# Performance work log

Hardware: AMD Instinct MI355X
Metric: run time of the kernel (lower is better)

## Reference

```python
import jax, jax.numpy as jnp
import numpy as np

F_THRESHOLD = 10  # zero out DCT coefficients with i + j <= 10 (low-frequency triangle)


def _dct_mat(N):
    # torch_dct.dct with norm=None: X_k = 2 * sum_n x_n cos(pi*(2n+1)*k/(2N))
    n = np.arange(N)
    k = np.arange(N)[:, None]
    return (2.0 * np.cos(np.pi * (2 * n + 1) * k / (2 * N))).astype(np.float32)  # [k, n]


def _idct_mat(N):
    # inverse of the norm=None DCT-II above: x_n = (1/N) * sum_k w_k X_k cos(pi*(2n+1)*k/(2N)), w_0=0.5
    n = np.arange(N)[:, None]
    k = np.arange(N)
    w = np.ones(N, dtype=np.float64)
    w[0] = 0.5
    return ((w * np.cos(np.pi * (2 * n + 1) * k / (2 * N))) / N).astype(np.float32)  # [n, k]


def _filtermask(H, W):
    i = jnp.arange(H)[:, None]
    j = jnp.arange(W)[None, :]
    return jnp.where(i + j <= F_THRESHOLD, 0.0, 1.0).astype(jnp.float32)  # [H, W]


def setup_inputs() -> dict:
    key = jax.random.key(0)
    im = jax.random.normal(key, (32, 3, 512, 512), dtype=jnp.float32)
    return {"im": im}


def reference(im) -> jnp.ndarray:
    B, C, H, W = im.shape
    Ch = jnp.asarray(_dct_mat(H))   # [kh, h]
    Cw = jnp.asarray(_dct_mat(W))   # [kw, w]
    Dh = jnp.asarray(_idct_mat(H))  # [h, kh]
    Dw = jnp.asarray(_idct_mat(W))  # [w, kw]
    mask = _filtermask(H, W)

    # dct_2d: DCT-II along W then along H
    x = jnp.einsum('kh,bchw,lw->bckl', Ch, im, Cw)
    x = x * mask  # zero low-frequency triangle
    # idct_2d
    x = jnp.einsum('hk,bckl,wl->bchw', Dh, x, Dw)
    return x
```

## Files before the change

### kernel.cpp

```cpp
#include <hip/hip_runtime.h>
#include <math.h>

#define NPIX 512
#define NK 11
#define NKP 12
#define NPAIR 121
#define RBLKS 8
#define NCH 96

typedef float vfloat4 __attribute__((ext_vector_type(4)));

#if __has_builtin(__builtin_amdgcn_cosf)
__device__ inline float cos_rev(float rev) { return __builtin_amdgcn_cosf(rev); }
#else
__device__ inline float cos_rev(float rev) { return __cosf(rev * 6.28318530717958647692f); }
#endif

__device__ inline float ctab(int h, int k) {
    int m = ((2 * h + 1) * k) & 2047;
    return 2.0f * cos_rev((float)m * (1.0f / 2048.0f));
}

#if __has_builtin(__builtin_amdgcn_update_dpp)
template <int CTRL>
__device__ inline float dpp_add(float x) {
    int xi = __builtin_bit_cast(int, x);
    int yi = __builtin_amdgcn_update_dpp(0, xi, CTRL, 0xf, 0xf, false);
    return x + __builtin_bit_cast(float, yi);
}
__device__ inline float red16(float x) {
    x = dpp_add<0x128>(x);
    x = dpp_add<0x124>(x);
    x = dpp_add<0x122>(x);
    x = dpp_add<0x121>(x);
    return x;
}
#else
__device__ inline float red16(float x) {
    x += __shfl_xor(x, 8);
    x += __shfl_xor(x, 4);
    x += __shfl_xor(x, 2);
    x += __shfl_xor(x, 1);
    return x;
}
#endif

__device__ inline void build_Cs64(float (*Cs64)[NKP], int t, int row0) {
#pragma unroll
    for (int j = 0; j < 3; ++j) {
        int idx = j * 256 + t;
        int hl = idx / NKP;
        int kk = idx - hl * NKP;
        Cs64[hl][kk] = (kk < NK) ? ctab(row0 + hl, kk) : 0.f;
    }
}

#define FMA4(ACC, CC) ACC.x += (CC) * v.x; ACC.y += (CC) * v.y; ACC.z += (CC) * v.z; ACC.w += (CC) * v.w;
#define DOT4(ACC) ((ACC).x * cl0 + (ACC).y * cl1 + (ACC).z * cl2 + (ACC).w * cl3)

__global__ __launch_bounds__(256, 4) void k_partial(const float* __restrict__ im,
                                                    float* __restrict__ plow) {
    __shared__ float Cs64[64][NKP];
    __shared__ float red[16][NPAIR];

    int bid = blockIdx.x;
    int c = bid >> 3, rb = bid & 7;
    int t = threadIdx.x;
    int row0 = rb * 64;

    build_Cs64(Cs64, t, row0);
    __syncthreads();

    int half = t >> 7;
    int col4 = t & 127;
    int w0 = col4 * 4;
    int hbase = half * 32;
    const float* imc = im + (size_t)c * NPIX * NPIX + (size_t)(row0 + hbase) * NPIX + w0;

    float4 z = make_float4(0.f, 0.f, 0.f, 0.f);
    float4 a0 = z, a1 = z, a2 = z, a3 = z, a4 = z, a5 = z, a6 = z, a7 = z, a8 = z, a9 = z, a10 = z;

#pragma unroll 4
    for (int i = 0; i < 32; ++i) {
        float4 v = *(const float4*)(imc + (size_t)i * NPIX);
        const float4* crow = (const float4*)&Cs64[hbase + i][0];
        float4 c0 = crow[0], c1 = crow[1], c2 = crow[2];
        FMA4(a0, c0.x) FMA4(a1, c0.y) FMA4(a2, c0.z) FMA4(a3, c0.w)
        FMA4(a4, c1.x) FMA4(a5, c1.y) FMA4(a6, c1.z) FMA4(a7, c1.w)
        FMA4(a8, c2.x) FMA4(a9, c2.y) FMA4(a10, c2.z)
    }

    int g = t >> 4;
    for (int l = 0; l < NK; ++l) {
        float cl0 = ctab(w0 + 0, l);
        float cl1 = ctab(w0 + 1, l);
        float cl2 = ctab(w0 + 2, l);
        float cl3 = ctab(w0 + 3, l);
        float p0 = red16(DOT4(a0));
        float p1 = red16(DOT4(a1));
        float p2 = red16(DOT4(a2));
        float p3 = red16(DOT4(a3));
        float p4 = red16(DOT4(a4));
        float p5 = red16(DOT4(a5));
        float p6 = red16(DOT4(a6));
        float p7 = red16(DOT4(a7));
        float p8 = red16(DOT4(a8));
        float p9 = red16(DOT4(a9));
        float p10 = red16(DOT4(a10));
        if ((t & 15) == 0) {
            red[g][0 * NK + l] = p0;  red[g][1 * NK + l] = p1;  red[g][2 * NK + l] = p2;
            red[g][3 * NK + l] = p3;  red[g][4 * NK + l] = p4;  red[g][5 * NK + l] = p5;
            red[g][6 * NK + l] = p6;  red[g][7 * NK + l] = p7;  red[g][8 * NK + l] = p8;
            red[g][9 * NK + l] = p9;  red[g][10 * NK + l] = p10;
        }
    }
    __syncthreads();

    if (t < NPAIR) {
        float s = 0.f;
#pragma unroll
        for (int gg = 0; gg < 16; ++gg) s += red[gg][t];
        plow[(size_t)bid * NPAIR + t] = s;
    }
}

__global__ __launch_bounds__(256, 2) void k_output(const float* __restrict__ im,
                                                   const float* __restrict__ plow,
                                                   float* __restrict__ out) {
    __shared__ float Cs64[64][NKP];
    __shared__ float Ls[NPAIR];

    int bid = blockIdx.x;
    int c = bid >> 3, rb = bid & 7;
    int t = threadIdx.x;
    int row0 = rb * 64;

    build_Cs64(Cs64, t, row0);

    if (t < NPAIR) {
        int k = t / NK, l = t % NK;
        float s = 0.f;
        const float* pp = plow + (size_t)c * RBLKS * NPAIR + t;
#pragma unroll
        for (int b = 0; b < RBLKS; ++b) s += pp[b * NPAIR];
        float sk = (k == 0 ? 0.5f : 1.0f) * (1.0f / 1024.0f);
        float sl = (l == 0 ? 0.5f : 1.0f) * (1.0f / 1024.0f);
        Ls[t] = (k + l <= 10) ? s * sk * sl : 0.f;
    }
    __syncthreads();

    int half = t >> 7;
    int col4 = t & 127;
    int w0 = col4 * 4;
    int hbase = half * 32;

    float4 z = make_float4(0.f, 0.f, 0.f, 0.f);
    float4 B0 = z, B1 = z, B2 = z, B3 = z, B4 = z, B5 = z, B6 = z, B7 = z, B8 = z, B9 = z, B10 = z;

#define BADD(BK, KI) { float lw = Ls[(KI) * NK + l]; BK.x += lw * cl0; BK.y += lw * cl1; BK.z += lw * cl2; BK.w += lw * cl3; }
    for (int l = 0; l < NK; ++l) {
        float cl0 = ctab(w0 + 0, l);
        float cl1 = ctab(w0 + 1, l);
        float cl2 = ctab(w0 + 2, l);
        float cl3 = ctab(w0 + 3, l);
        BADD(B0, 0) BADD(B1, 1) BADD(B2, 2) BADD(B3, 3) BADD(B4, 4) BADD(B5, 5)
        BADD(B6, 6) BADD(B7, 7) BADD(B8, 8) BADD(B9, 9) BADD(B10, 10)
    }

    const float* imc = im + (size_t)c * NPIX * NPIX + (size_t)(row0 + hbase) * NPIX + w0;
    float* outc = out + (size_t)c * NPIX * NPIX + (size_t)(row0 + hbase) * NPIX + w0;

#define CORR(comp) (c0.x * B0.comp + c0.y * B1.comp + c0.z * B2.comp + c0.w * B3.comp \
                  + c1.x * B4.comp + c1.y * B5.comp + c1.z * B6.comp + c1.w * B7.comp \
                  + c2.x * B8.comp + c2.y * B9.comp + c2.z * B10.comp)

#pragma unroll 4
    for (int i = 0; i < 32; ++i) {
        float4 v = *(const float4*)(imc + (size_t)i * NPIX);
        const float4* crow = (const float4*)&Cs64[hbase + i][0];
        float4 c0 = crow[0], c1 = crow[1], c2 = crow[2];
        vfloat4 o;
        o.x = v.x - CORR(x);
        o.y = v.y - CORR(y);
        o.z = v.z - CORR(z);
        o.w = v.w - CORR(w);
#if __has_builtin(__builtin_nontemporal_store)
        __builtin_nontemporal_store(o, (vfloat4*)(outc + (size_t)i * NPIX));
#else
        *(vfloat4*)(outc + (size_t)i * NPIX) = o;
#endif
    }
}

extern "C" void kernel_launch(void* const* d_in, const int* in_sizes, int n_in,
                              void* d_out, int out_size, void* d_ws, size_t ws_size,
                              hipStream_t stream) {
    const float* im = (const float*)d_in[0];
    float* out = (float*)d_out;
    float* plow = (float*)d_ws;

    k_partial<<<NCH * RBLKS, 256, 0, stream>>>(im, plow);
    k_output<<<NCH * RBLKS, 256, 0, stream>>>(im, plow, out);
}
```

Before: 61.05 us.

## Fuse partial-sum and output kernels with per-channel atomic counter barrier

```diff
diff --git a/kernel.cpp b/kernel.cpp
--- a/kernel.cpp
+++ b/kernel.cpp
@@ -58,10 +58,13 @@
 #define FMA4(ACC, CC) ACC.x += (CC) * v.x; ACC.y += (CC) * v.y; ACC.z += (CC) * v.z; ACC.w += (CC) * v.w;
 #define DOT4(ACC) ((ACC).x * cl0 + (ACC).y * cl1 + (ACC).z * cl2 + (ACC).w * cl3)
 
-__global__ __launch_bounds__(256, 4) void k_partial(const float* __restrict__ im,
-                                                    float* __restrict__ plow) {
+__global__ __launch_bounds__(256, 4) void k_fused(const float* __restrict__ im,
+                                                  float* __restrict__ plow,
+                                                  int* __restrict__ cnt,
+                                                  float* __restrict__ out) {
     __shared__ float Cs64[64][NKP];
     __shared__ float red[16][NPAIR];
+    __shared__ float Ls[NPAIR];
 
     int bid = blockIdx.x;
     int c = bid >> 3, rb = bid & 7;
@@ -77,85 +80,87 @@
     int hbase = half * 32;
     const float* imc = im + (size_t)c * NPIX * NPIX + (size_t)(row0 + hbase) * NPIX + w0;
 
-    float4 z = make_float4(0.f, 0.f, 0.f, 0.f);
-    float4 a0 = z, a1 = z, a2 = z, a3 = z, a4 = z, a5 = z, a6 = z, a7 = z, a8 = z, a9 = z, a10 = z;
+    {
+        float4 z = make_float4(0.f, 0.f, 0.f, 0.f);
+        float4 a0 = z, a1 = z, a2 = z, a3 = z, a4 = z, a5 = z, a6 = z, a7 = z,
+               a8 = z, a9 = z, a10 = z;
 
 #pragma unroll 4
-    for (int i = 0; i < 32; ++i) {
-        float4 v = *(const float4*)(imc + (size_t)i * NPIX);
-        const float4* crow = (const float4*)&Cs64[hbase + i][0];
-        float4 c0 = crow[0], c1 = crow[1], c2 = crow[2];
-        FMA4(a0, c0.x) FMA4(a1, c0.y) FMA4(a2, c0.z) FMA4(a3, c0.w)
-        FMA4(a4, c1.x) FMA4(a5, c1.y) FMA4(a6, c1.z) FMA4(a7, c1.w)
-        FMA4(a8, c2.x) FMA4(a9, c2.y) FMA4(a10, c2.z)
-    }
-
-    int g = t >> 4;
-    for (int l = 0; l < NK; ++l) {
-        float cl0 = ctab(w0 + 0, l);
-        float cl1 = ctab(w0 + 1, l);
-        float cl2 = ctab(w0 + 2, l);
-        float cl3 = ctab(w0 + 3, l);
-        float p0 = red16(DOT4(a0));
-        float p1 = red16(DOT4(a1));
-        float p2 = red16(DOT4(a2));
-        float p3 = red16(DOT4(a3));
-        float p4 = red16(DOT4(a4));
-        float p5 = red16(DOT4(a5));
-        float p6 = red16(DOT4(a6));
-        float p7 = red16(DOT4(a7));
-        float p8 = red16(DOT4(a8));
-        float p9 = red16(DOT4(a9));
-        float p10 = red16(DOT4(a10));
-        if ((t & 15) == 0) {
-            red[g][0 * NK + l] = p0;  red[g][1 * NK + l] = p1;  red[g][2 * NK + l] = p2;
-            red[g][3 * NK + l] = p3;  red[g][4 * NK + l] = p4;  red[g][5 * NK + l] = p5;
-            red[g][6 * NK + l] = p6;  red[g][7 * NK + l] = p7;  red[g][8 * NK + l] = p8;
-            red[g][9 * NK + l] = p9;  red[g][10 * NK + l] = p10;
+        for (int i = 0; i < 32; ++i) {
+            float4 v = *(const float4*)(imc + (size_t)i * NPIX);
+            const float4* crow = (const float4*)&Cs64[hbase + i][0];
+            float4 c0 = crow[0], c1 = crow[1], c2 = crow[2];
+            FMA4(a0, c0.x) FMA4(a1, c0.y) FMA4(a2, c0.z) FMA4(a3, c0.w)
+            FMA4(a4, c1.x) FMA4(a5, c1.y) FMA4(a6, c1.z) FMA4(a7, c1.w)
+            FMA4(a8, c2.x) FMA4(a9, c2.y) FMA4(a10, c2.z)
+        }
+
+        int g = t >> 4;
+        for (int l = 0; l < NK; ++l) {
+            float cl0 = ctab(w0 + 0, l);
+            float cl1 = ctab(w0 + 1, l);
+            float cl2 = ctab(w0 + 2, l);
+            float cl3 = ctab(w0 + 3, l);
+            float p0 = red16(DOT4(a0));
+            float p1 = red16(DOT4(a1));
+            float p2 = red16(DOT4(a2));
+            float p3 = red16(DOT4(a3));
+            float p4 = red16(DOT4(a4));
+            float p5 = red16(DOT4(a5));
+            float p6 = red16(DOT4(a6));
+            float p7 = red16(DOT4(a7));
+            float p8 = red16(DOT4(a8));
+            float p9 = red16(DOT4(a9));
+            float p10 = red16(DOT4(a10));
+            if ((t & 15) == 0) {
+                red[g][0 * NK + l] = p0;  red[g][1 * NK + l] = p1;  red[g][2 * NK + l] = p2;
+                red[g][3 * NK + l] = p3;  red[g][4 * NK + l] = p4;  red[g][5 * NK + l] = p5;
+                red[g][6 * NK + l] = p6;  red[g][7 * NK + l] = p7;  red[g][8 * NK + l] = p8;
+                red[g][9 * NK + l] = p9;  red[g][10 * NK + l] = p10;
+            }
+        }
+        __syncthreads();
+
+        if (t < NPAIR) {
+            float s = 0.f;
+#pragma unroll
+            for (int gg = 0; gg < 16; ++gg) s += red[gg][t];
+            __hip_atomic_store(&plow[(size_t)bid * NPAIR + t], s,
+                               __ATOMIC_RELAXED, __HIP_MEMORY_SCOPE_AGENT);
+        }
+        __syncthreads();
+
+        if (t == 0) {
+            __hip_atomic_fetch_add(&cnt[c], 1, __ATOMIC_RELEASE,
+                                   __HIP_MEMORY_SCOPE_AGENT);
+        }
+    }
+
+    if (t == 0) {
+        while (__hip_atomic_load(&cnt[c], __ATOMIC_ACQUIRE,
+                                 __HIP_MEMORY_SCOPE_AGENT) < RBLKS) {
+            __builtin_amdgcn_s_sleep(8);
         }
     }
     __syncthreads();
-
-    if (t < NPAIR) {
-        float s = 0.f;
-#pragma unroll
-        for (int gg = 0; gg < 16; ++gg) s += red[gg][t];
-        plow[(size_t)bid * NPAIR + t] = s;
-    }
-}
-
-__global__ __launch_bounds__(256, 2) void k_output(const float* __restrict__ im,
-                                                   const float* __restrict__ plow,
-                                                   float* __restrict__ out) {
-    __shared__ float Cs64[64][NKP];
-    __shared__ float Ls[NPAIR];
-
-    int bid = blockIdx.x;
-    int c = bid >> 3, rb = bid & 7;
-    int t = threadIdx.x;
-    int row0 = rb * 64;
-
-    build_Cs64(Cs64, t, row0);
 
     if (t < NPAIR) {
         int k = t / NK, l = t % NK;
         float s = 0.f;
         const float* pp = plow + (size_t)c * RBLKS * NPAIR + t;
 #pragma unroll
-        for (int b = 0; b < RBLKS; ++b) s += pp[b * NPAIR];
+        for (int b = 0; b < RBLKS; ++b)
+            s += __hip_atomic_load(&pp[b * NPAIR], __ATOMIC_RELAXED,
+                                   __HIP_MEMORY_SCOPE_AGENT);
         float sk = (k == 0 ? 0.5f : 1.0f) * (1.0f / 1024.0f);
         float sl = (l == 0 ? 0.5f : 1.0f) * (1.0f / 1024.0f);
         Ls[t] = (k + l <= 10) ? s * sk * sl : 0.f;
     }
     __syncthreads();
 
-    int half = t >> 7;
-    int col4 = t & 127;
-    int w0 = col4 * 4;
-    int hbase = half * 32;
-
     float4 z = make_float4(0.f, 0.f, 0.f, 0.f);
-    float4 B0 = z, B1 = z, B2 = z, B3 = z, B4 = z, B5 = z, B6 = z, B7 = z, B8 = z, B9 = z, B10 = z;
+    float4 B0 = z, B1 = z, B2 = z, B3 = z, B4 = z, B5 = z, B6 = z, B7 = z,
+           B8 = z, B9 = z, B10 = z;
 
 #define BADD(BK, KI) { float lw = Ls[(KI) * NK + l]; BK.x += lw * cl0; BK.y += lw * cl1; BK.z += lw * cl2; BK.w += lw * cl3; }
     for (int l = 0; l < NK; ++l) {
@@ -167,7 +172,6 @@
         BADD(B6, 6) BADD(B7, 7) BADD(B8, 8) BADD(B9, 9) BADD(B10, 10)
     }
 
-    const float* imc = im + (size_t)c * NPIX * NPIX + (size_t)(row0 + hbase) * NPIX + w0;
     float* outc = out + (size_t)c * NPIX * NPIX + (size_t)(row0 + hbase) * NPIX + w0;
 
 #define CORR(comp) (c0.x * B0.comp + c0.y * B1.comp + c0.z * B2.comp + c0.w * B3.comp \
@@ -198,7 +202,8 @@
     const float* im = (const float*)d_in[0];
     float* out = (float*)d_out;
     float* plow = (float*)d_ws;
-
-    k_partial<<<NCH * RBLKS, 256, 0, stream>>>(im, plow);
-    k_output<<<NCH * RBLKS, 256, 0, stream>>>(im, plow, out);
-}
+    int* cnt = (int*)((char*)d_ws + 372224);
+
+    hipMemsetAsync(cnt, 0, NCH * sizeof(int), stream);
+    k_fused<<<NCH * RBLKS, 256, 0, stream>>>(im, plow, cnt, out);
+}
```

Result: slower. 106.5 us (+74.5%).
